# Kernel tuning notes

Hardware: AMD Instinct MI355X
Metric: run time of the kernel (lower is better)

Reference implementation:

```python
import jax, jax.numpy as jnp
import numpy as np

H = 8        # heads
DH = 64      # dim_head
K = 16       # num_neighbors
EMB = 512    # emb_dim
INNER = H * DH
AINNER = 4 * DH  # per-head attn_mlp hidden width
POSH = 64


def setup_inputs() -> dict:
    key = jax.random.key(0)
    ks = jax.random.split(key, 20)
    bs, n = 2, 1024
    rn = lambda k, s, sc=1.0: jax.random.normal(k, s, jnp.float32) * sc
    return {
        "query": rn(ks[0], (bs, n, EMB)),
        "key_in": rn(ks[1], (bs, n, EMB)),
        "value": rn(ks[2], (bs, n, EMB)),
        "canonical": rn(ks[3], (bs, n, 3)),
        "w_q": rn(ks[4], (EMB, INNER), EMB ** -0.5),
        "w_k": rn(ks[5], (EMB, INNER), EMB ** -0.5),
        "w_v": rn(ks[6], (EMB, INNER), EMB ** -0.5),
        "w_out": rn(ks[7], (INNER, EMB), INNER ** -0.5),
        "b_out": rn(ks[8], (EMB,), 0.02),
        "pos_w1": rn(ks[9], (3, POSH), 3 ** -0.5),
        "pos_b1": rn(ks[10], (POSH,), 0.02),
        "pos_w2": rn(ks[11], (POSH, INNER), POSH ** -0.5),
        "pos_b2": rn(ks[12], (INNER,), 0.02),
        "aw1": rn(ks[13], (H, AINNER, DH), DH ** -0.5),   # grouped conv1 weight per head: (out=4*DH, in=DH)
        "ab1": rn(ks[14], (H, AINNER), 0.02),
        "aw2": rn(ks[15], (H, DH, AINNER), AINNER ** -0.5),  # grouped conv2: (out=DH, in=4*DH)
        "ab2": rn(ks[16], (H, DH), 0.02),
    }


def reference(query, key_in, value, canonical, w_q, w_k, w_v, w_out, b_out,
              pos_w1, pos_b1, pos_w2, pos_b2, aw1, ab1, aw2, ab2):
    bs, n, _ = query.shape
    # projections, then b n (h d) -> b h n d
    to_heads = lambda t: t.reshape(bs, n, H, DH).transpose(0, 2, 1, 3)
    q = to_heads(query @ w_q)
    k = to_heads(key_in @ w_k)
    v = to_heads(value @ w_v)

    # KNN on canonical coords: (b,n,n) squared distances, k smallest (includes self)
    d2 = jnp.sum((canonical[:, :, None, :] - canonical[:, None, :, :]) ** 2, axis=-1)
    _, nbr = jax.lax.top_k(-d2, K)                       # (b,n,K)
    idx = (nbr + (jnp.arange(bs) * n)[:, None, None]).reshape(-1)  # flat rows into bs*n

    # relative position embedding
    pos_nn = canonical.reshape(bs * n, 3)[idx].reshape(bs, n, K, 3)
    rel = pos_nn - canonical[:, :, None, :]
    rpe = jax.nn.relu(rel @ pos_w1 + pos_b1) @ pos_w2 + pos_b2        # (b,n,K,inner)
    rpe = rpe.reshape(bs, n, K, H, DH).transpose(0, 3, 1, 2, 4)       # (b,h,i,j,d)

    # faithful replication of the original view(bs*n,-1)[idx] gathers on (b,h,n,d) tensors
    gather = lambda t: t.reshape(bs * n, -1)[idx].reshape(bs, H, n, K, DH)
    qg, kg, vg = gather(q), gather(k), gather(v)
    vg = vg + rpe
    x = (qg - kg) + rpe                                  # (b,h,i,j,d)

    # grouped 1x1 conv attn_mlp == per-head MLP over d
    hdn = jax.nn.relu(jnp.einsum('bhijd,hed->bhije', x, aw1) + ab1[None, :, None, None, :])
    sim = jnp.einsum('bhije,hde->bhijd', hdn, aw2) + ab2[None, :, None, None, :]

    attn = jax.nn.softmax(sim, axis=3)                   # softmax over neighbors j
    norm = jnp.sqrt(jnp.sum(attn * attn, axis=2, keepdims=True))  # F.normalize over i
    attn = attn / jnp.maximum(norm, 1e-12)

    agg = jnp.einsum('bhijd,bhijd->bhid', attn, vg)      # (b,h,i,d)
    agg = agg.transpose(0, 2, 1, 3).reshape(bs, n, INNER)
    return agg @ w_out + b_out
```

## Files before the change

### kernel.cpp

```cpp
#include <hip/hip_runtime.h>


#define BS 2
#define NPT 1024
#define HH 8
#define DH 64
#define KNN 16
#define EMB 512
#define INNER 512
#define AINNER 256
#define POSH 64

typedef unsigned short u16;
typedef unsigned int u32;
typedef __attribute__((ext_vector_type(8))) short bf16x8;
typedef __attribute__((ext_vector_type(4))) float f32x4;

__device__ __forceinline__ float bf2f(u16 b) { union { u32 u; float f; } v; v.u = ((u32)b) << 16; return v.f; }
__device__ __forceinline__ u16 f2bf_rne(float f) {
    u32 x = __float_as_uint(f);
    u32 r = x + 0x7fffu + ((x >> 16) & 1u);
    return (u16)(r >> 16);
}
__device__ __forceinline__ void split2(float f, u16& hi, u16& lo) {
    u32 bits = __float_as_uint(f);
    hi = (u16)(bits >> 16);
    float resid = f - __uint_as_float(bits & 0xffff0000u);
    lo = (u16)(__float_as_uint(resid) >> 16);
}

__global__ __launch_bounds__(256) void k_pre(const float* __restrict__ query,
                                             const float* __restrict__ key_in,
                                             const float* __restrict__ value,
                                             const float* __restrict__ aw1,
                                             const float* __restrict__ aw2,
                                             const float* __restrict__ pw2,
                                             u16* __restrict__ qhi, u16* __restrict__ qlo,
                                             u16* __restrict__ khi, u16* __restrict__ klo,
                                             u16* __restrict__ vhi, u16* __restrict__ vlo,
                                             u16* __restrict__ w1hi, u16* __restrict__ w2hi,
                                             u16* __restrict__ rw2hi)
{
    const int bx = blockIdx.x, t = threadIdx.x;
    if (bx < 3072) {
        const int m = bx >> 10;
        const int v = (((bx & 1023) * 256) + t) * 4;
        const float* src; u16* dh; u16* dl;
        switch (m) {
            case 0:  src = query;  dh = qhi; dl = qlo; break;
            case 1:  src = key_in; dh = khi; dl = klo; break;
            default: src = value;  dh = vhi; dl = vlo; break;
        }
        float4 f = *(const float4*)&src[v];
        if (m == 1) { f.x = -f.x; f.y = -f.y; f.z = -f.z; f.w = -f.w; }
        ushort4 h4, l4;
        split2(f.x, h4.x, l4.x); split2(f.y, h4.y, l4.y);
        split2(f.z, h4.z, l4.z); split2(f.w, h4.w, l4.w);
        *(ushort4*)&dh[v] = h4;
        *(ushort4*)&dl[v] = l4;
    } else {
        int idx = (bx - 3072) * 256 + t;
        if (idx < 131072) {
            w1hi[idx] = f2bf_rne(aw1[idx]);
        } else if (idx < 262144) {
            int k2 = idx - 131072;
            w2hi[k2] = f2bf_rne(aw2[k2]);
        } else {
            int k2 = idx - 262144;
            int p = k2 & 63; int hd = k2 >> 6;
            int h = hd >> 6; int d = hd & 63;
            rw2hi[k2] = f2bf_rne(pw2[(size_t)p * INNER + h * DH + d]);
        }
    }
}

__global__ __launch_bounds__(256) void k_split_T(const float* __restrict__ wq,
                                                 const float* __restrict__ wk,
                                                 const float* __restrict__ wv,
                                                 const float* __restrict__ wout,
                                                 u16* __restrict__ o0h, u16* __restrict__ o0l,
                                                 u16* __restrict__ o1h, u16* __restrict__ o1l,
                                                 u16* __restrict__ o2h, u16* __restrict__ o2l,
                                                 u16* __restrict__ o3h, u16* __restrict__ o3l)
{
    __shared__ float S[64][65];
    const int t = threadIdx.x;
    const int e0 = blockIdx.x * 64, c0 = blockIdx.y * 64;
    const float* src; u16* dh; u16* dl;
    switch (blockIdx.z) {
        case 0:  src = wq;   dh = o0h; dl = o0l; break;
        case 1:  src = wk;   dh = o1h; dl = o1l; break;
        case 2:  src = wv;   dh = o2h; dl = o2l; break;
        default: src = wout; dh = o3h; dl = o3l; break;
    }
    #pragma unroll
    for (int s = 0; s < 16; ++s) {
        int v = s * 256 + t; int r = v >> 6, c = v & 63;
        S[r][c] = src[(size_t)(e0 + r) * 512 + c0 + c];
    }
    __syncthreads();
    #pragma unroll
    for (int s = 0; s < 16; ++s) {
        int v = s * 256 + t; int c = v >> 6, e = v & 63;
        u16 hi, lo; split2(S[e][c], hi, lo);
        size_t off = (size_t)(c0 + c) * 512 + e0 + e;
        dh[off] = hi; dl[off] = lo;
    }
}

__global__ __launch_bounds__(256) void k_projM(const u16* __restrict__ qhi, const u16* __restrict__ qlo,
                                               const u16* __restrict__ khi, const u16* __restrict__ klo,
                                               const u16* __restrict__ vhi, const u16* __restrict__ vlo,
                                               const u16* __restrict__ wqh, const u16* __restrict__ wql,
                                               const u16* __restrict__ wkh, const u16* __restrict__ wkl,
                                               const u16* __restrict__ wvh, const u16* __restrict__ wvl,
                                               float* __restrict__ Dws, float* __restrict__ Vws)
{
    __shared__ u16 S[12][64 * 40];
    const int t = threadIdx.x, l = t & 63, w = t >> 6;
    const int lm = l & 15, lg = (l >> 4) * 8;
    const int g0 = blockIdx.x * 64, c0 = blockIdx.y * 64;
    const int sr = t >> 2, sc = (t & 3) * 8;

    f32x4 accD[4] = {{0,0,0,0},{0,0,0,0},{0,0,0,0},{0,0,0,0}};
    f32x4 accV[4] = {{0,0,0,0},{0,0,0,0},{0,0,0,0},{0,0,0,0}};

    for (int ks = 0; ks < 16; ++ks) {
        const int k0 = ks * 32;
        if (ks) __syncthreads();
        #define STG(p, base, rb) \
            *(uint4*)&S[p][sr * 40 + sc] = *(const uint4*)&(base)[(size_t)((rb) + sr) * 512 + k0 + sc];
        STG(0, qhi, g0) STG(1, qlo, g0) STG(2, khi, g0) STG(3, klo, g0)
        STG(4, vhi, g0) STG(5, vlo, g0)
        STG(6, wqh, c0) STG(7, wql, c0) STG(8, wkh, c0) STG(9, wkl, c0)
        STG(10, wvh, c0) STG(11, wvl, c0)
        #undef STG
        __syncthreads();

        const int ao = (w * 16 + lm) * 40 + lg;
        bf16x8 aqh = *(const bf16x8*)&S[0][ao];
        bf16x8 aql = *(const bf16x8*)&S[1][ao];
        bf16x8 akh = *(const bf16x8*)&S[2][ao];
        bf16x8 akl = *(const bf16x8*)&S[3][ao];
        bf16x8 avh = *(const bf16x8*)&S[4][ao];
        bf16x8 avl = *(const bf16x8*)&S[5][ao];
        #pragma unroll
        for (int ct = 0; ct < 4; ++ct) {
            const int bo = (ct * 16 + lm) * 40 + lg;
            bf16x8 bqh = *(const bf16x8*)&S[6][bo];
            bf16x8 bql = *(const bf16x8*)&S[7][bo];
            bf16x8 bkh = *(const bf16x8*)&S[8][bo];
            bf16x8 bkl = *(const bf16x8*)&S[9][bo];
            bf16x8 bvh = *(const bf16x8*)&S[10][bo];
            bf16x8 bvl = *(const bf16x8*)&S[11][bo];
            accD[ct] = __builtin_amdgcn_mfma_f32_16x16x32_bf16(aqh, bqh, accD[ct], 0, 0, 0);
            accD[ct] = __builtin_amdgcn_mfma_f32_16x16x32_bf16(aql, bqh, accD[ct], 0, 0, 0);
            accD[ct] = __builtin_amdgcn_mfma_f32_16x16x32_bf16(aqh, bql, accD[ct], 0, 0, 0);
            accD[ct] = __builtin_amdgcn_mfma_f32_16x16x32_bf16(akh, bkh, accD[ct], 0, 0, 0);
            accD[ct] = __builtin_amdgcn_mfma_f32_16x16x32_bf16(akl, bkh, accD[ct], 0, 0, 0);
            accD[ct] = __builtin_amdgcn_mfma_f32_16x16x32_bf16(akh, bkl, accD[ct], 0, 0, 0);
            accV[ct] = __builtin_amdgcn_mfma_f32_16x16x32_bf16(avh, bvh, accV[ct], 0, 0, 0);
            accV[ct] = __builtin_amdgcn_mfma_f32_16x16x32_bf16(avl, bvh, accV[ct], 0, 0, 0);
            accV[ct] = __builtin_amdgcn_mfma_f32_16x16x32_bf16(avh, bvl, accV[ct], 0, 0, 0);
        }
    }

    const int b = blockIdx.x >> 4;
    const int h = blockIdx.y;
    #pragma unroll
    for (int ct = 0; ct < 4; ++ct) {
        #pragma unroll
        for (int r = 0; r < 4; ++r) {
            int g = g0 + w * 16 + (l >> 4) * 4 + r;
            int i = g & 1023;
            size_t off = (((size_t)(b * HH + h)) * NPT + i) * DH + ct * 16 + lm;
            Dws[off] = accD[ct][r];
            Vws[off] = accV[ct][r];
        }
    }
}

__global__ __launch_bounds__(256) void k_knn(const float* __restrict__ canonical, int* __restrict__ nbr)
{
    const int t = threadIdx.x, l = t & 63, w = t >> 6;
    const int i = blockIdx.x * 4 + w;
    const int b = blockIdx.y;
    const float* cb = canonical + (size_t)b * NPT * 3;
    const float qx = cb[i*3+0], qy = cb[i*3+1], qz = cb[i*3+2];
    float d2v[16];
    #pragma unroll
    for (int k = 0; k < 16; ++k) {
        int j = l * 16 + k;
        float dx = __fsub_rn(cb[j*3+0], qx);
        float dy = __fsub_rn(cb[j*3+1], qy);
        float dz = __fsub_rn(cb[j*3+2], qz);
        d2v[k] = __fadd_rn(__fadd_rn(__fmul_rn(dx,dx), __fmul_rn(dy,dy)), __fmul_rn(dz,dz));
    }
    unsigned alive = 0xFFFFu;
    int* out = nbr + ((size_t)b * NPT + i) * KNN;
    for (int sel = 0; sel < KNN; ++sel) {
        float bv = __builtin_inff(); int bk = 16;
        #pragma unroll
        for (int k = 0; k < 16; ++k) {
            float v = ((alive >> k) & 1u) ? d2v[k] : __builtin_inff();
            if (v < bv) { bv = v; bk = k; }
        }
        int bj = l * 16 + bk;
        #pragma unroll
        for (int m = 32; m >= 1; m >>= 1) {
            float ov = __shfl_xor(bv, m, 64);
            int   oj = __shfl_xor(bj, m, 64);
            if (ov < bv || (ov == bv && oj < bj)) { bv = ov; bj = oj; }
        }
        if (l == 0) out[sel] = bj;
        if ((bj >> 4) == l) alive &= ~(1u << (bj & 15));
    }
}

__global__ __launch_bounds__(256, 3) void k_attn(const float* __restrict__ Dws,
                                              const float* __restrict__ Vws,
                                              const float* __restrict__ canonical,
                                              const int* __restrict__ nbr,
                                              const float* __restrict__ pw1,
                                              const float* __restrict__ pb1,
                                              const float* __restrict__ pb2,
                                              const float* __restrict__ ab1,
                                              const float* __restrict__ ab2,
                                              const u16* __restrict__ w1hi,
                                              const u16* __restrict__ w2hi,
                                              const u16* __restrict__ rw2hi,
                                              u16* __restrict__ vvb,
                                              u16* __restrict__ attnb,
                                              float* __restrict__ npart2)
{
    const int it = blockIdx.x, h = blockIdx.y, b = blockIdx.z, t = threadIdx.x;
    const int l = t & 63, w = t >> 6;
    const int lm = l & 15, lg = (l >> 4) * 8;
    const int dd = w * 16 + lm;

    __shared__ u16 h1s[2][16 * 72];
    __shared__ u16 Xs[2][16 * 72];
    __shared__ u16 Hs[2][16 * 264];
    __shared__ u16 rw2s[64 * 72];
    __shared__ float pw1s[3 * POSH];
    __shared__ float pb1s[POSH];
    __shared__ float rel_all[8][KNN][3];
    __shared__ int nbrrow[KNN];

    bf16x8 w1f[8], w2f[8];
    float b1v[4];
    #pragma unroll
    for (int q = 0; q < 4; ++q) {
        int e = (w * 4 + q) * 16 + lm;
        b1v[q] = ab1[h * AINNER + e];
        #pragma unroll
        for (int kc = 0; kc < 2; ++kc)
            w1f[q*2+kc] = *(const bf16x8*)&w1hi[((size_t)(h * AINNER + e)) * DH + kc * 32 + lg];
    }
    const float b2v  = ab2[h * DH + dd];
    const float pb2v = pb2[h * DH + dd];
    #pragma unroll
    for (int kc = 0; kc < 8; ++kc)
        w2f[kc] = *(const bf16x8*)&w2hi[((size_t)(h * DH + dd)) * AINNER + kc * 32 + lg];

    for (int v = t; v < 64 * 64; v += 256) {
        int d = v >> 6, p = v & 63;
        rw2s[d * 72 + p] = rw2hi[(h * DH + d) * POSH + p];
    }
    if (t < 192) pw1s[t] = pw1[t];
    if (t < 64)  pb1s[t] = pb1[t];
    if (t < KNN) nbrrow[t] = nbr[((size_t)b * NPT + h * 128 + it) * KNN + t];
    if (t < 128) {
        int ti = t >> 4, jj = t & 15;
        int i2 = it * 8 + ti;
        int nv2 = nbr[((size_t)b * NPT + i2) * KNN + jj];
        const float* cn = canonical + ((size_t)b * NPT + nv2) * 3;
        const float* ci = canonical + ((size_t)b * NPT + i2) * 3;
        rel_all[ti][jj][0] = cn[0] - ci[0];
        rel_all[ti][jj][1] = cn[1] - ci[1];
        rel_all[ti][jj][2] = cn[2] - ci[2];
    }
    __syncthreads();

    float dvp[2][4], vwp[2][4];
    auto gather = [&](int pp) {
        #pragma unroll
        for (int u = 0; u < 2; ++u) {
            const int ti = 2 * pp + u;
            #pragma unroll
            for (int r = 0; r < 4; ++r) {
                int j = (l >> 4) * 4 + r;
                int nv = nbrrow[2 * ti + (j >> 3)];
                size_t off = (((size_t)b * HH + (nv >> 7)) * NPT + (nv & 127) * 8 + (j & 7)) * DH + dd;
                dvp[u][r] = Dws[off];
                vwp[u][r] = Vws[off];
            }
        }
    };
    gather(0);

    float npacc[4] = {0.f, 0.f, 0.f, 0.f};

    for (int p = 0; p < 4; ++p) {
        #pragma unroll
        for (int u = 0; u < 2; ++u) {
            const int ti = 2 * p + u;
            #pragma unroll
            for (int r = 0; r < 4; ++r) {
                int v = r * 256 + t; int j = v >> 6; int pp = v & 63;
                float a = pb1s[pp];
                a = fmaf(rel_all[ti][j][0], pw1s[pp], a);
                a = fmaf(rel_all[ti][j][1], pw1s[64 + pp], a);
                a = fmaf(rel_all[ti][j][2], pw1s[128 + pp], a);
                h1s[u][j * 72 + pp] = f2bf_rne(fmaxf(a, 0.0f));
            }
        }
        __syncthreads();
        #pragma unroll
        for (int u = 0; u < 2; ++u) {
            const int i = it * 8 + 2 * p + u;
            f32x4 racc = {0.f, 0.f, 0.f, 0.f};
            #pragma unroll
            for (int kc = 0; kc < 2; ++kc) {
                bf16x8 ah = *(const bf16x8*)&h1s[u][lm * 72 + kc * 32 + lg];
                bf16x8 rb = *(const bf16x8*)&rw2s[dd * 72 + kc * 32 + lg];
                racc = __builtin_amdgcn_mfma_f32_16x16x32_bf16(ah, rb, racc, 0, 0, 0);
            }
            u16* vvrow = vvb + (((size_t)(b * HH + h) * NPT + i) * KNN) * DH + dd;
            #pragma unroll
            for (int r = 0; r < 4; ++r) {
                int j = (l >> 4) * 4 + r;
                float rp = racc[r] + pb2v;
                Xs[u][j * 72 + dd] = f2bf_rne(dvp[u][r] + rp);
                vvrow[j * DH] = f2bf_rne(vwp[u][r] + rp);
            }
        }
        if (p < 3) gather(p + 1);
        __syncthreads();
        #pragma unroll
        for (int u = 0; u < 2; ++u) {
            f32x4 acc1[4] = {{0,0,0,0},{0,0,0,0},{0,0,0,0},{0,0,0,0}};
            #pragma unroll
            for (int kc = 0; kc < 2; ++kc) {
                bf16x8 ah = *(const bf16x8*)&Xs[u][lm * 72 + kc * 32 + lg];
                #pragma unroll
                for (int q = 0; q < 4; ++q)
                    acc1[q] = __builtin_amdgcn_mfma_f32_16x16x32_bf16(ah, w1f[q*2+kc], acc1[q], 0, 0, 0);
            }
            #pragma unroll
            for (int q = 0; q < 4; ++q) {
                int ee = (w * 4 + q) * 16 + lm;
                #pragma unroll
                for (int r = 0; r < 4; ++r) {
                    int jj = (l >> 4) * 4 + r;
                    Hs[u][jj * 264 + ee] = f2bf_rne(fmaxf(acc1[q][r] + b1v[q], 0.0f));
                }
            }
        }
        __syncthreads();
        #pragma unroll
        for (int u = 0; u < 2; ++u) {
            const int i = it * 8 + 2 * p + u;
            f32x4 acc2[4] = {{0,0,0,0},{0,0,0,0},{0,0,0,0},{0,0,0,0}};
            #pragma unroll
            for (int kc = 0; kc < 8; ++kc) {
                bf16x8 ah = *(const bf16x8*)&Hs[u][lm * 264 + kc * 32 + lg];
                acc2[kc & 3] = __builtin_amdgcn_mfma_f32_16x16x32_bf16(ah, w2f[kc], acc2[kc & 3], 0, 0, 0);
            }
            float sim[4];
            #pragma unroll
            for (int r = 0; r < 4; ++r)
                sim[r] = ((acc2[0][r] + acc2[1][r]) + (acc2[2][r] + acc2[3][r])) + b2v;
            float m = fmaxf(fmaxf(sim[0], sim[1]), fmaxf(sim[2], sim[3]));
            m = fmaxf(m, __shfl_xor(m, 16, 64));
            m = fmaxf(m, __shfl_xor(m, 32, 64));
            float ex[4], s = 0.0f;
            #pragma unroll
            for (int r = 0; r < 4; ++r) { ex[r] = __expf(sim[r] - m); s += ex[r]; }
            s += __shfl_xor(s, 16, 64);
            s += __shfl_xor(s, 32, 64);
            float inv = 1.0f / s;
            u16* ao = attnb + (((size_t)(b * HH + h) * NPT + i) * KNN) * DH + dd;
            #pragma unroll
            for (int r = 0; r < 4; ++r) {
                u16 abf16 = f2bf_rne(ex[r] * inv);
                ao[((l >> 4) * 4 + r) * DH] = abf16;
                float abf = bf2f(abf16);
                npacc[r] = fmaf(abf, abf, npacc[r]);
            }
        }
    }

    float* np = npart2 + ((size_t)((b * HH + h) * 128 + it)) * 1024 + ((l >> 4) * 4) * 64 + dd;
    #pragma unroll
    for (int r = 0; r < 4; ++r) np[r * 64] = npacc[r];
}

__global__ __launch_bounds__(256) void k_normR(const float* __restrict__ npart2, float* __restrict__ nrm)
{
    int v = blockIdx.x * 256 + threadIdx.x;
    int bh = v >> 10, jd = v & 1023;
    const float* src = npart2 + (size_t)bh * 128 * 1024 + jd;
    float s = 0.0f;
    for (int it2 = 0; it2 < 128; ++it2) s += src[(size_t)it2 * 1024];
    nrm[v] = sqrtf(s);
}

__global__ __launch_bounds__(256) void k_agg(const u16* __restrict__ attnb,
                                             const float* __restrict__ nrm,
                                             const u16* __restrict__ vvb,
                                             u16* __restrict__ agghi,
                                             u16* __restrict__ agglo)
{
    const int it = blockIdx.x, h = blockIdx.y, b = blockIdx.z, t = threadIdx.x;
    const int d = t & 63, si = t >> 6;
    const int i = it * 4 + si;
    __shared__ float rn[KNN * DH];
    for (int v = t; v < KNN * DH; v += 256)
        rn[v] = 1.0f / fmaxf(nrm[(size_t)(b * HH + h) * 1024 + v], 1e-12f);
    __syncthreads();
    const u16* ab = attnb + (((size_t)(b * HH + h) * NPT + i) * KNN) * DH + d;
    const u16* vb = vvb   + (((size_t)(b * HH + h) * NPT + i) * KNN) * DH + d;
    float acc = 0.0f;
    #pragma unroll
    for (int j = 0; j < KNN; ++j) {
        float a  = bf2f(ab[j * DH]);
        float vv = bf2f(vb[j * DH]);
        acc = fmaf(a * rn[j * DH + d], vv, acc);
    }
    size_t off = ((size_t)b * NPT + i) * INNER + h * DH + d;
    u16 hi, lo; split2(acc, hi, lo);
    agghi[off] = hi;
    agglo[off] = lo;
}

__global__ __launch_bounds__(256) void k_outM(const u16* __restrict__ agghi, const u16* __restrict__ agglo,
                                              const u16* __restrict__ wth, const u16* __restrict__ wtl,
                                              const float* __restrict__ bout,
                                              float* __restrict__ outp)
{
    __shared__ u16 S[4][64 * 40];
    const int t = threadIdx.x, l = t & 63, w = t >> 6;
    const int lm = l & 15, lg = (l >> 4) * 8;
    const int g0 = blockIdx.x * 64, c0 = blockIdx.y * 64;
    const int sr = t >> 2, sc = (t & 3) * 8;

    f32x4 acc[4] = {{0,0,0,0},{0,0,0,0},{0,0,0,0},{0,0,0,0}};
    float bv4[4];
    #pragma unroll
    for (int ct = 0; ct < 4; ++ct) bv4[ct] = bout[c0 + ct * 16 + lm];

    for (int ks = 0; ks < 16; ++ks) {
        const int k0 = ks * 32;
        if (ks) __syncthreads();
        *(uint4*)&S[0][sr * 40 + sc] = *(const uint4*)&agghi[(size_t)(g0 + sr) * 512 + k0 + sc];
        *(uint4*)&S[1][sr * 40 + sc] = *(const uint4*)&agglo[(size_t)(g0 + sr) * 512 + k0 + sc];
        *(uint4*)&S[2][sr * 40 + sc] = *(const uint4*)&wth[(size_t)(c0 + sr) * 512 + k0 + sc];
        *(uint4*)&S[3][sr * 40 + sc] = *(const uint4*)&wtl[(size_t)(c0 + sr) * 512 + k0 + sc];
        __syncthreads();

        const int ao = (w * 16 + lm) * 40 + lg;
        bf16x8 ah = *(const bf16x8*)&S[0][ao];
        bf16x8 al = *(const bf16x8*)&S[1][ao];
        #pragma unroll
        for (int ct = 0; ct < 4; ++ct) {
            const int bo = (ct * 16 + lm) * 40 + lg;
            bf16x8 bh = *(const bf16x8*)&S[2][bo];
            bf16x8 bl = *(const bf16x8*)&S[3][bo];
            acc[ct] = __builtin_amdgcn_mfma_f32_16x16x32_bf16(ah, bh, acc[ct], 0, 0, 0);
            acc[ct] = __builtin_amdgcn_mfma_f32_16x16x32_bf16(al, bh, acc[ct], 0, 0, 0);
            acc[ct] = __builtin_amdgcn_mfma_f32_16x16x32_bf16(ah, bl, acc[ct], 0, 0, 0);
        }
    }
    #pragma unroll
    for (int ct = 0; ct < 4; ++ct) {
        #pragma unroll
        for (int r = 0; r < 4; ++r) {
            int g = g0 + w * 16 + (l >> 4) * 4 + r;
            outp[(size_t)g * 512 + c0 + ct * 16 + lm] = acc[ct][r] + bv4[ct];
        }
    }
}

extern "C" void kernel_launch(void* const* d_in, const int* in_sizes, int n_in,
                              void* d_out, int out_size, void* d_ws, size_t ws_size,
                              hipStream_t stream) {
    const float* query     = (const float*)d_in[0];
    const float* key_in    = (const float*)d_in[1];
    const float* value     = (const float*)d_in[2];
    const float* canonical = (const float*)d_in[3];
    const float* wq   = (const float*)d_in[4];
    const float* wk   = (const float*)d_in[5];
    const float* wv   = (const float*)d_in[6];
    const float* wout = (const float*)d_in[7];
    const float* bout = (const float*)d_in[8];
    const float* pw1  = (const float*)d_in[9];
    const float* pb1  = (const float*)d_in[10];
    const float* pw2  = (const float*)d_in[11];
    const float* pb2  = (const float*)d_in[12];
    const float* aw1  = (const float*)d_in[13];
    const float* ab1  = (const float*)d_in[14];
    const float* aw2  = (const float*)d_in[15];
    const float* ab2  = (const float*)d_in[16];

    float* ws    = (float*)d_ws;
    float* Dws   = ws;
    float* Vws   = ws + 1048576;
    float* aggp  = ws + 2097152;
    float* nrm   = ws + 3162112;
    int*   nbr   = (int*)(ws + 3293184);
    float* attnR = ws + 3325952;

    u16* agghi = (u16*)aggp;
    u16* agglo = agghi + 1048576;

    u16* attnb = (u16*)attnR;
    u16* pl   = (u16*)(attnR + 8388608);
    u16* qhi  = pl;                u16* qlo  = pl + 1048576;
    u16* khi  = pl + 2097152;      u16* klo  = pl + 3145728;
    u16* vhi  = pl + 4194304;      u16* vlo  = pl + 5242880;
    u16* wqTh = pl + 6291456;      u16* wqTl = pl + 6553600;
    u16* wkTh = pl + 6815744;      u16* wkTl = pl + 7077888;
    u16* wvTh = pl + 7340032;      u16* wvTl = pl + 7602176;
    float* npart2 = attnR + 12582912;

    u16* u16b  = (u16*)(ws + 20103168);
    u16* w1hi  = u16b;
    u16* w2hi  = u16b + 262144;
    u16* rw2hi = u16b + 524288;
    u16* vvb   = u16b + 589824;
    u16* wouTh = u16b + 17367040;
    u16* wouTl = u16b + 17629184;

    k_pre<<<4224, 256, 0, stream>>>(query, key_in, value, aw1, aw2, pw2,
                                    qhi, qlo, khi, klo, vhi, vlo, w1hi, w2hi, rw2hi);
    k_split_T<<<dim3(8, 8, 4), 256, 0, stream>>>(wq, wk, wv, wout,
                                                 wqTh, wqTl, wkTh, wkTl, wvTh, wvTl, wouTh, wouTl);
    k_projM<<<dim3(32, 8), 256, 0, stream>>>(qhi, qlo, khi, klo, vhi, vlo,
                                             wqTh, wqTl, wkTh, wkTl, wvTh, wvTl, Dws, Vws);
    k_knn<<<dim3(256, BS), 256, 0, stream>>>(canonical, nbr);
    k_attn<<<dim3(128, HH, BS), 256, 0, stream>>>(Dws, Vws, canonical, nbr, pw1, pb1, pb2,
                                                  ab1, ab2, w1hi, w2hi, rw2hi, vvb, attnb, npart2);
    k_normR<<<64, 256, 0, stream>>>(npart2, nrm);
    k_agg<<<dim3(256, HH, BS), 256, 0, stream>>>(attnb, nrm, vvb, agghi, agglo);
    k_outM<<<dim3(32, 8), 256, 0, stream>>>(agghi, agglo, wouTh, wouTl, bout, (float*)d_out);
}
```

Before: 153.1 us.

## Fuse input hi/lo split into projection GEMM and vectorize aggregation kernel

The separate pre-pass that split query/key/value into bf16 hi/lo planes is removed. The projection GEMM now loads fp32 inputs directly, negates key, and splits into LDS, which avoids writing and re-reading about 12 MB of intermediate planes. The aggregation kernel is rewritten so each wavefront handles one point with 16-byte vector loads of attention and value rows, then reduces across neighbors with cross-lane shuffles. In exchange, each GEMM block redoes the split for its A tile across 8 column blocks, adding redundant conversion work.

New measurement: 152.4 us. About the same (-0.5%).

```diff
diff --git a/kernel.cpp b/kernel.cpp
--- a/kernel.cpp
+++ b/kernel.cpp
@@ -28,49 +28,28 @@
     float resid = f - __uint_as_float(bits & 0xffff0000u);
     lo = (u16)(__float_as_uint(resid) >> 16);
 }
-
-__global__ __launch_bounds__(256) void k_pre(const float* __restrict__ query,
-                                             const float* __restrict__ key_in,
-                                             const float* __restrict__ value,
-                                             const float* __restrict__ aw1,
+__device__ __forceinline__ void split4(float4 f, ushort4& h, ushort4& l) {
+    split2(f.x, h.x, l.x); split2(f.y, h.y, l.y);
+    split2(f.z, h.z, l.z); split2(f.w, h.w, l.w);
+}
+
+__global__ __launch_bounds__(256) void k_pre(const float* __restrict__ aw1,
                                              const float* __restrict__ aw2,
                                              const float* __restrict__ pw2,
-                                             u16* __restrict__ qhi, u16* __restrict__ qlo,
-                                             u16* __restrict__ khi, u16* __restrict__ klo,
-                                             u16* __restrict__ vhi, u16* __restrict__ vlo,
                                              u16* __restrict__ w1hi, u16* __restrict__ w2hi,
                                              u16* __restrict__ rw2hi)
 {
-    const int bx = blockIdx.x, t = threadIdx.x;
-    if (bx < 3072) {
-        const int m = bx >> 10;
-        const int v = (((bx & 1023) * 256) + t) * 4;
-        const float* src; u16* dh; u16* dl;
-        switch (m) {
-            case 0:  src = query;  dh = qhi; dl = qlo; break;
-            case 1:  src = key_in; dh = khi; dl = klo; break;
-            default: src = value;  dh = vhi; dl = vlo; break;
-        }
-        float4 f = *(const float4*)&src[v];
-        if (m == 1) { f.x = -f.x; f.y = -f.y; f.z = -f.z; f.w = -f.w; }
-        ushort4 h4, l4;
-        split2(f.x, h4.x, l4.x); split2(f.y, h4.y, l4.y);
-        split2(f.z, h4.z, l4.z); split2(f.w, h4.w, l4.w);
-        *(ushort4*)&dh[v] = h4;
-        *(ushort4*)&dl[v] = l4;
+    int idx = blockIdx.x * 256 + threadIdx.x;
+    if (idx < 131072) {
+        w1hi[idx] = f2bf_rne(aw1[idx]);
+    } else if (idx < 262144) {
+        int k2 = idx - 131072;
+        w2hi[k2] = f2bf_rne(aw2[k2]);
     } else {
-        int idx = (bx - 3072) * 256 + t;
-        if (idx < 131072) {
-            w1hi[idx] = f2bf_rne(aw1[idx]);
-        } else if (idx < 262144) {
-            int k2 = idx - 131072;
-            w2hi[k2] = f2bf_rne(aw2[k2]);
-        } else {
-            int k2 = idx - 262144;
-            int p = k2 & 63; int hd = k2 >> 6;
-            int h = hd >> 6; int d = hd & 63;
-            rw2hi[k2] = f2bf_rne(pw2[(size_t)p * INNER + h * DH + d]);
-        }
+        int k2 = idx - 262144;
+        int p = k2 & 63; int hd = k2 >> 6;
+        int h = hd >> 6; int d = hd & 63;
+        rw2hi[k2] = f2bf_rne(pw2[(size_t)p * INNER + h * DH + d]);
     }
 }
 
@@ -108,9 +87,9 @@
     }
 }
 
-__global__ __launch_bounds__(256) void k_projM(const u16* __restrict__ qhi, const u16* __restrict__ qlo,
-                                               const u16* __restrict__ khi, const u16* __restrict__ klo,
-                                               const u16* __restrict__ vhi, const u16* __restrict__ vlo,
+__global__ __launch_bounds__(256) void k_projM(const float* __restrict__ qf,
+                                               const float* __restrict__ kf,
+                                               const float* __restrict__ vf,
                                                const u16* __restrict__ wqh, const u16* __restrict__ wql,
                                                const u16* __restrict__ wkh, const u16* __restrict__ wkl,
                                                const u16* __restrict__ wvh, const u16* __restrict__ wvl,
@@ -125,15 +104,31 @@
     f32x4 accD[4] = {{0,0,0,0},{0,0,0,0},{0,0,0,0},{0,0,0,0}};
     f32x4 accV[4] = {{0,0,0,0},{0,0,0,0},{0,0,0,0},{0,0,0,0}};
 
+    const float* asrc0 = qf; const float* asrc1 = kf; const float* asrc2 = vf;
+
     for (int ks = 0; ks < 16; ++ks) {
         const int k0 = ks * 32;
         if (ks) __syncthreads();
-        #define STG(p, base, rb) \
-            *(uint4*)&S[p][sr * 40 + sc] = *(const uint4*)&(base)[(size_t)((rb) + sr) * 512 + k0 + sc];
-        STG(0, qhi, g0) STG(1, qlo, g0) STG(2, khi, g0) STG(3, klo, g0)
-        STG(4, vhi, g0) STG(5, vlo, g0)
-        STG(6, wqh, c0) STG(7, wql, c0) STG(8, wkh, c0) STG(9, wkl, c0)
-        STG(10, wvh, c0) STG(11, wvl, c0)
+        #pragma unroll
+        for (int m = 0; m < 3; ++m) {
+            const float* sp = (m == 0 ? asrc0 : (m == 1 ? asrc1 : asrc2))
+                              + (size_t)(g0 + sr) * 512 + k0 + sc;
+            float4 f0 = *(const float4*)sp;
+            float4 f1 = *(const float4*)(sp + 4);
+            if (m == 1) {
+                f0.x = -f0.x; f0.y = -f0.y; f0.z = -f0.z; f0.w = -f0.w;
+                f1.x = -f1.x; f1.y = -f1.y; f1.z = -f1.z; f1.w = -f1.w;
+            }
+            ushort4 h0, l0, h1, l1;
+            split4(f0, h0, l0); split4(f1, h1, l1);
+            *(ushort4*)&S[2*m  ][sr * 40 + sc]     = h0;
+            *(ushort4*)&S[2*m  ][sr * 40 + sc + 4] = h1;
+            *(ushort4*)&S[2*m+1][sr * 40 + sc]     = l0;
+            *(ushort4*)&S[2*m+1][sr * 40 + sc + 4] = l1;
+        }
+        #define STG(p, base) \
+            *(uint4*)&S[p][sr * 40 + sc] = *(const uint4*)&(base)[(size_t)(c0 + sr) * 512 + k0 + sc];
+        STG(6, wqh) STG(7, wql) STG(8, wkh) STG(9, wkl) STG(10, wvh) STG(11, wvl)
         #undef STG
         __syncthreads();
 
@@ -413,25 +408,46 @@
                                              u16* __restrict__ agglo)
 {
     const int it = blockIdx.x, h = blockIdx.y, b = blockIdx.z, t = threadIdx.x;
-    const int d = t & 63, si = t >> 6;
-    const int i = it * 4 + si;
+    const int l = t & 63, w = t >> 6;
+    const int i = it * 4 + w;
     __shared__ float rn[KNN * DH];
     for (int v = t; v < KNN * DH; v += 256)
         rn[v] = 1.0f / fmaxf(nrm[(size_t)(b * HH + h) * 1024 + v], 1e-12f);
     __syncthreads();
-    const u16* ab = attnb + (((size_t)(b * HH + h) * NPT + i) * KNN) * DH + d;
-    const u16* vb = vvb   + (((size_t)(b * HH + h) * NPT + i) * KNN) * DH + d;
-    float acc = 0.0f;
-    #pragma unroll
-    for (int j = 0; j < KNN; ++j) {
-        float a  = bf2f(ab[j * DH]);
-        float vv = bf2f(vb[j * DH]);
-        acc = fmaf(a * rn[j * DH + d], vv, acc);
-    }
-    size_t off = ((size_t)b * NPT + i) * INNER + h * DH + d;
-    u16 hi, lo; split2(acc, hi, lo);
-    agghi[off] = hi;
-    agglo[off] = lo;
+    const size_t row = ((size_t)(b * HH + h) * NPT + i) * (KNN * DH);
+    bf16x8 a0 = *(const bf16x8*)&attnb[row + l * 8];
+    bf16x8 a1 = *(const bf16x8*)&attnb[row + 512 + l * 8];
+    bf16x8 q0 = *(const bf16x8*)&vvb[row + l * 8];
+    bf16x8 q1 = *(const bf16x8*)&vvb[row + 512 + l * 8];
+    const int dbase = (l & 7) * 8;
+    float4 ra = *(const float4*)&rn[(l >> 3) * 64 + dbase];
+    float4 rb = *(const float4*)&rn[(l >> 3) * 64 + dbase + 4];
+    float4 rc = *(const float4*)&rn[(8 + (l >> 3)) * 64 + dbase];
+    float4 rd = *(const float4*)&rn[(8 + (l >> 3)) * 64 + dbase + 4];
+    const float r0[8] = {ra.x, ra.y, ra.z, ra.w, rb.x, rb.y, rb.z, rb.w};
+    const float r1[8] = {rc.x, rc.y, rc.z, rc.w, rd.x, rd.y, rd.z, rd.w};
+    float acc[8];
+    #pragma unroll
+    for (int e = 0; e < 8; ++e)
+        acc[e] = bf2f((u16)a0[e]) * r0[e] * bf2f((u16)q0[e])
+               + bf2f((u16)a1[e]) * r1[e] * bf2f((u16)q1[e]);
+    #pragma unroll
+    for (int mask = 8; mask <= 32; mask <<= 1)
+        #pragma unroll
+        for (int e = 0; e < 8; ++e)
+            acc[e] += __shfl_xor(acc[e], mask, 64);
+    if (l < 8) {
+        size_t off = ((size_t)b * NPT + i) * INNER + h * DH + l * 8;
+        ushort4 h0, l0, h1, l1;
+        split2(acc[0], h0.x, l0.x); split2(acc[1], h0.y, l0.y);
+        split2(acc[2], h0.z, l0.z); split2(acc[3], h0.w, l0.w);
+        split2(acc[4], h1.x, l1.x); split2(acc[5], h1.y, l1.y);
+        split2(acc[6], h1.z, l1.z); split2(acc[7], h1.w, l1.w);
+        *(ushort4*)&agghi[off]     = h0;
+        *(ushort4*)&agghi[off + 4] = h1;
+        *(ushort4*)&agglo[off]     = l0;
+        *(ushort4*)&agglo[off + 4] = l1;
+    }
 }
 
 __global__ __launch_bounds__(256) void k_outM(const u16* __restrict__ agghi, const u16* __restrict__ agglo,
@@ -516,12 +532,9 @@
 
     u16* attnb = (u16*)attnR;
     u16* pl   = (u16*)(attnR + 8388608);
-    u16* qhi  = pl;                u16* qlo  = pl + 1048576;
-    u16* khi  = pl + 2097152;      u16* klo  = pl + 3145728;
-    u16* vhi  = pl + 4194304;      u16* vlo  = pl + 5242880;
-    u16* wqTh = pl + 6291456;      u16* wqTl = pl + 6553600;
-    u16* wkTh = pl + 6815744;      u16* wkTl = pl + 7077888;
-    u16* wvTh = pl + 7340032;      u16* wvTl = pl + 7602176;
+    u16* wqTh = pl;                u16* wqTl = pl + 262144;
+    u16* wkTh = pl + 524288;       u16* wkTl = pl + 786432;
+    u16* wvTh = pl + 1048576;      u16* wvTl = pl + 1310720;
     float* npart2 = attnR + 12582912;
 
     u16* u16b  = (u16*)(ws + 20103168);
@@ -532,11 +545,10 @@
     u16* wouTh = u16b + 17367040;
     u16* wouTl = u16b + 17629184;
 
-    k_pre<<<4224, 256, 0, stream>>>(query, key_in, value, aw1, aw2, pw2,
-                                    qhi, qlo, khi, klo, vhi, vlo, w1hi, w2hi, rw2hi);
+    k_pre<<<1152, 256, 0, stream>>>(aw1, aw2, pw2, w1hi, w2hi, rw2hi);
     k_split_T<<<dim3(8, 8, 4), 256, 0, stream>>>(wq, wk, wv, wout,
                                                  wqTh, wqTl, wkTh, wkTl, wvTh, wvTl, wouTh, wouTl);
-    k_projM<<<dim3(32, 8), 256, 0, stream>>>(qhi, qlo, khi, klo, vhi, vlo,
+    k_projM<<<dim3(32, 8), 256, 0, stream>>>(query, key_in, value,
                                              wqTh, wqTl, wkTh, wkTl, wvTh, wvTl, Dws, Vws);
     k_knn<<<dim3(256, BS), 256, 0, stream>>>(canonical, nbr);
     k_attn<<<dim3(128, HH, BS), 256, 0, stream>>>(Dws, Vws, canonical, nbr, pw1, pb1, pb2,
```
